# Optimization experiments

Measured on AMD Instinct MI355X. Metric: run time of the kernel, lower is better.

Reference implementation:

```python
import jax, jax.numpy as jnp
import numpy as np

QMAX = 127.0  # int8 symmetric range


def _quantize(t):
    # per-tensor symmetric int8 quantization
    scale = jnp.maximum(jnp.max(jnp.abs(t)) / QMAX, 1e-8)
    q = jnp.clip(jnp.round(t / scale), -QMAX, QMAX)
    return q, scale


def setup_inputs() -> dict:
    key = jax.random.key(0)
    kx, kw, kb = jax.random.split(key, 3)
    x = jax.random.normal(kx, (32, 128, 56, 56), dtype=jnp.float32)
    weight = jax.random.normal(kw, (256, 128, 3, 3), dtype=jnp.float32) * 0.05
    bias = jax.random.normal(kb, (256,), dtype=jnp.float32) * 0.05
    return {"x": x, "weight": weight, "bias": bias}


def reference(x, weight, bias):
    # Quantize activations and weights to int8 grid (values held in fp32;
    # products are exact small integers, matching int32 GEMM accumulation).
    qx, sx = _quantize(x)
    qw, sw = _quantize(weight)
    # im2col GEMM conv == standard conv on quantized values, int accumulate.
    acc = jax.lax.conv_general_dilated(
        qx, qw,
        window_strides=(1, 1),
        padding=((1, 1), (1, 1)),
        rhs_dilation=(1, 1),
        dimension_numbers=("NCHW", "OIHW", "NCHW"),
    )
    # Dequantize and add bias.
    out = acc * (sx * sw) + bias[None, :, None, None]
    return out
```

## Files before the change

### kernel.cpp

```cpp
#include <hip/hip_runtime.h>
#include <hip/hip_bf16.h>


typedef int v4i __attribute__((ext_vector_type(4)));

#define NBATCH 32
#define CIN    128
#define HW     56
#define PIX    (HW*HW)
#define COUT   256
#define XTOT   (NBATCH*CIN*PIX)
#define WTOT   (COUT*CIN*9)

template <int ITERS>
__global__ __launch_bounds__(256) void absmax_part_kernel(
    const float* __restrict__ in, float* __restrict__ partial)
{
    const float4* in4 = (const float4*)in;
    const int t      = blockIdx.x * 256 + threadIdx.x;
    const int stride = gridDim.x * 256;
    float m = 0.f;
#pragma unroll
    for (int k = 0; k < ITERS; ++k) {
        float4 v = in4[t + k * stride];
        m = fmaxf(m, fmaxf(fmaxf(fabsf(v.x), fabsf(v.y)),
                           fmaxf(fabsf(v.z), fabsf(v.w))));
    }
#pragma unroll
    for (int off = 32; off >= 1; off >>= 1)
        m = fmaxf(m, __shfl_xor(m, off, 64));
    __shared__ float wmax[4];
    const int lane = threadIdx.x & 63, wid = threadIdx.x >> 6;
    if (lane == 0) wmax[wid] = m;
    __syncthreads();
    if (threadIdx.x == 0)
        partial[blockIdx.x] =
            fmaxf(fmaxf(wmax[0], wmax[1]), fmaxf(wmax[2], wmax[3]));
}

__global__ __launch_bounds__(256) void finalize_kernel(
    const float* __restrict__ px, const float* __restrict__ pw,
    float* __restrict__ scales)
{
    const int tid = threadIdx.x;
    float mxv = 0.f, mwv = 0.f;
#pragma unroll
    for (int k = 0; k < 7; ++k)
        mxv = fmaxf(mxv, px[k * 256 + tid]);
    if (tid < 72) mwv = pw[tid];
#pragma unroll
    for (int off = 32; off >= 1; off >>= 1) {
        mxv = fmaxf(mxv, __shfl_xor(mxv, off, 64));
        mwv = fmaxf(mwv, __shfl_xor(mwv, off, 64));
    }
    __shared__ float sx[4], sw[4];
    const int lane = tid & 63, wid = tid >> 6;
    if (lane == 0) { sx[wid] = mxv; sw[wid] = mwv; }
    __syncthreads();
    if (tid == 0) {
        float fx = fmaxf(fmaxf(sx[0], sx[1]), fmaxf(sx[2], sx[3]));
        float fw = fmaxf(fmaxf(sw[0], sw[1]), fmaxf(sw[2], sw[3]));
        scales[0] = fmaxf(fx / 127.0f, 1e-8f);
        scales[1] = fmaxf(fw / 127.0f, 1e-8f);
    }
}

__global__ void quant_w_kernel(const float* __restrict__ w,
                               const float* __restrict__ scales,
                               signed char* __restrict__ qw) {
    float s = scales[1];
    int idx = blockIdx.x * blockDim.x + threadIdx.x;
    if (idx >= WTOT) return;
    int o   = idx / (CIN * 9);
    int rem = idx % (CIN * 9);
    int c   = rem / 9;
    int khw = rem % 9;
    float q = rintf(w[idx] / s);
    q = fminf(127.0f, fmaxf(-127.0f, q));
    qw[khw * (COUT * CIN) + o * CIN + c] = (signed char)(int)q;
}

__global__ __launch_bounds__(256) void quant_x_kernel(const float* __restrict__ x,
                                                      const float* __restrict__ scales,
                                                      signed char* __restrict__ qx) {
    __shared__ signed char lds[32 * 132];
    float s = scales[0];
    const int n   = blockIdx.y;
    const int p0  = blockIdx.x * 32;
    const int tid = threadIdx.x;
#pragma unroll
    for (int i = 0; i < 4; ++i) {
        int idx = i * 256 + tid;
        int c   = idx >> 3;
        int pq  = idx & 7;
        float4 v = *(const float4*)&x[((size_t)(n * CIN + c)) * PIX + p0 + pq * 4];
        float qv[4] = {v.x, v.y, v.z, v.w};
#pragma unroll
        for (int j = 0; j < 4; ++j) {
            float q = rintf(qv[j] / s);
            q = fminf(127.0f, fmaxf(-127.0f, q));
            lds[(pq * 4 + j) * 132 + c] = (signed char)(int)q;
        }
    }
    __syncthreads();
#pragma unroll
    for (int i = 0; i < 4; ++i) {
        int idx = i * 256 + tid;
        int pp  = idx >> 5;
        int cw  = (idx & 31) * 4;
        *(int*)&qx[((size_t)(n * PIX + p0 + pp)) * CIN + cw] =
            *(const int*)&lds[pp * 132 + cw];
    }
}

__global__ __launch_bounds__(256, 4) void conv_kernel(
    const signed char* __restrict__ qx,
    const signed char* __restrict__ qw,
    const float* __restrict__ bias,
    const float* __restrict__ scales,
    float* __restrict__ out)
{
    __shared__ signed char lds[232 * 128];
    const int tid  = threadIdx.x;
    const int lane = tid & 63;
    const int wid  = tid >> 6;
    const int prow = lane & 15;
    const int klo  = lane >> 4;

    const int bid = blockIdx.x;
    const int nh  = bid & 1;
    const int mt  = bid >> 1;
    const int n   = mt / 49;
    const int p0  = (mt % 49) * 64;
    const int hbase = p0 / HW - 1;

    const size_t xbase = (size_t)n * PIX * CIN;

#pragma unroll
    for (int it = 0; it < 8; ++it) {
        int chunk = it * 256 + tid;
        if (chunk < 232 * 8) {
            int r  = chunk >> 3;
            int cb = (chunk & 7) * 16;
            int hr = r / 58;
            int wc = r - hr * 58;
            int h  = hbase + hr;
            int w  = wc - 1;
            bool valid = ((unsigned)h < HW) && ((unsigned)w < HW);
            int p = valid ? (h * HW + w) : 0;
            v4i v = *(const v4i*)(qx + xbase + (size_t)p * CIN + cb);
            if (!valid) v = (v4i){0, 0, 0, 0};
            *(v4i*)&lds[r * 128 + (cb ^ ((r & 7) << 4))] = v;
        }
    }
    __syncthreads();

    int rr[4];
#pragma unroll
    for (int s = 0; s < 4; ++s) {
        int p = p0 + s * 16 + prow;
        int h = p / HW, w = p - h * HW;
        rr[s] = (h - hbase) * 58 + (w + 1);
    }

    const int ch0     = nh * 128 + wid * 32;
    const int colbase = klo * 16;

    v4i acc[4][2] = {};

    const signed char* b0ptr = qw + (size_t)(ch0 + prow) * CIN + colbase;
#define BADDR(st) (b0ptr + (size_t)((st) >> 1) * (COUT * CIN) + ((st) & 1) * 64)

    v4i bcur0 = *(const v4i*)BADDR(0);
    v4i bcur1 = *(const v4i*)(BADDR(0) + 16 * CIN);

#pragma unroll
    for (int st = 0; st < 18; ++st) {
        v4i bn0 = bcur0, bn1 = bcur1;
        if (st < 17) {
            const signed char* bp = BADDR(st + 1);
            bn0 = *(const v4i*)bp;
            bn1 = *(const v4i*)(bp + 16 * CIN);
        }
        const int khw  = st >> 1;
        const int rofs = (khw / 3 - 1) * 58 + (khw % 3 - 1);
        const int col  = (st & 1) * 64 + colbase;
        v4i a[4];
#pragma unroll
        for (int s = 0; s < 4; ++s) {
            int r = rr[s] + rofs;
            a[s] = *(const v4i*)&lds[r * 128 + (col ^ ((r & 7) << 4))];
        }
#pragma unroll
        for (int s = 0; s < 4; ++s) {
            acc[s][0] = __builtin_amdgcn_mfma_i32_16x16x64_i8(a[s], bcur0, acc[s][0], 0, 0, 0);
            acc[s][1] = __builtin_amdgcn_mfma_i32_16x16x64_i8(a[s], bcur1, acc[s][1], 0, 0, 0);
        }
        bcur0 = bn0; bcur1 = bn1;
    }
#undef BADDR

    float s0 = scales[0], s1 = scales[1];
    asm volatile("" : "+v"(s0));
    const float comb = s0 * s1;
    const size_t obase = (size_t)n * COUT * PIX;
#pragma unroll
    for (int t = 0; t < 2; ++t) {
        int ch = ch0 + t * 16 + prow;
        float bs = bias[ch];
#pragma unroll
        for (int s = 0; s < 4; ++s) {
            int p = p0 + s * 16 + klo * 4;
            float4 v;
            v.x = (float)acc[s][t].x * comb + bs;
            v.y = (float)acc[s][t].y * comb + bs;
            v.z = (float)acc[s][t].z * comb + bs;
            v.w = (float)acc[s][t].w * comb + bs;
            *(float4*)&out[obase + (size_t)ch * PIX + p] = v;
        }
    }
}

extern "C" void kernel_launch(void* const* d_in, const int* in_sizes, int n_in,
                              void* d_out, int out_size, void* d_ws, size_t ws_size,
                              hipStream_t stream) {
    const float* x    = (const float*)d_in[0];
    const float* w    = (const float*)d_in[1];
    const float* bias = (const float*)d_in[2];
    float* out = (float*)d_out;

    float*       scales = (float*)d_ws;
    float*       px     = (float*)((char*)d_ws + 256);
    float*       pw     = (float*)((char*)d_ws + 7680);
    signed char* qx     = (signed char*)d_ws + 8192;
    signed char* qw     = qx + (size_t)XTOT;

    absmax_part_kernel<7><<<1792, 256, 0, stream>>>(x, px);
    absmax_part_kernel<4><<<72, 256, 0, stream>>>(w, pw);
    finalize_kernel<<<1, 256, 0, stream>>>(px, pw, scales);
    quant_w_kernel<<<WTOT / 256, 256, 0, stream>>>(w, scales, qw);
    quant_x_kernel<<<dim3(98, 32), 256, 0, stream>>>(x, scales, qx);
    conv_kernel<<<3136, 256, 0, stream>>>(qx, qw, bias, scales, out);
}
```

Baseline: 217.9 us.

## Widen conv tile to all 256 output channels and merge absmax launches

Each conv block now computes all 256 output channels for its 64-pixel tile instead of half, so the staged input halo in LDS is loaded once rather than twice and the grid halves. Blocks are remapped with a stride-8 swizzle across the 1568 tiles. The two absmax reductions are merged into one launch, saving a kernel launch. The wider tile doubles accumulator registers (16 MFMA accumulators per wave) and drops the B-operand software prefetch, which may cut occupancy under the 4-block launch bound and expose global load latency.

```diff
diff --git a/kernel.cpp b/kernel.cpp
--- a/kernel.cpp
+++ b/kernel.cpp
@@ -12,19 +12,32 @@
 #define XTOT   (NBATCH*CIN*PIX)
 #define WTOT   (COUT*CIN*9)
 
-template <int ITERS>
-__global__ __launch_bounds__(256) void absmax_part_kernel(
-    const float* __restrict__ in, float* __restrict__ partial)
+__global__ __launch_bounds__(256) void absmax_both_kernel(
+    const float* __restrict__ x, const float* __restrict__ w,
+    float* __restrict__ px, float* __restrict__ pw)
 {
-    const float4* in4 = (const float4*)in;
-    const int t      = blockIdx.x * 256 + threadIdx.x;
-    const int stride = gridDim.x * 256;
+    const int bid = blockIdx.x;
     float m = 0.f;
-#pragma unroll
-    for (int k = 0; k < ITERS; ++k) {
-        float4 v = in4[t + k * stride];
-        m = fmaxf(m, fmaxf(fmaxf(fabsf(v.x), fabsf(v.y)),
-                           fmaxf(fabsf(v.z), fabsf(v.w))));
+    if (bid < 1792) {
+        const float4* in4 = (const float4*)x;
+        const int t = bid * 256 + threadIdx.x;
+        const int stride = 1792 * 256;
+#pragma unroll
+        for (int k = 0; k < 7; ++k) {
+            float4 v = in4[t + k * stride];
+            m = fmaxf(m, fmaxf(fmaxf(fabsf(v.x), fabsf(v.y)),
+                               fmaxf(fabsf(v.z), fabsf(v.w))));
+        }
+    } else {
+        const float4* in4 = (const float4*)w;
+        const int t = (bid - 1792) * 256 + threadIdx.x;
+        const int stride = 72 * 256;
+#pragma unroll
+        for (int k = 0; k < 4; ++k) {
+            float4 v = in4[t + k * stride];
+            m = fmaxf(m, fmaxf(fmaxf(fabsf(v.x), fabsf(v.y)),
+                               fmaxf(fabsf(v.z), fabsf(v.w))));
+        }
     }
 #pragma unroll
     for (int off = 32; off >= 1; off >>= 1)
@@ -33,9 +46,10 @@
     const int lane = threadIdx.x & 63, wid = threadIdx.x >> 6;
     if (lane == 0) wmax[wid] = m;
     __syncthreads();
-    if (threadIdx.x == 0)
-        partial[blockIdx.x] =
-            fmaxf(fmaxf(wmax[0], wmax[1]), fmaxf(wmax[2], wmax[3]));
+    if (threadIdx.x == 0) {
+        float r = fmaxf(fmaxf(wmax[0], wmax[1]), fmaxf(wmax[2], wmax[3]));
+        if (bid < 1792) px[bid] = r; else pw[bid - 1792] = r;
+    }
 }
 
 __global__ __launch_bounds__(256) void finalize_kernel(
@@ -127,11 +141,9 @@
     const int prow = lane & 15;
     const int klo  = lane >> 4;
 
-    const int bid = blockIdx.x;
-    const int nh  = bid & 1;
-    const int mt  = bid >> 1;
-    const int n   = mt / 49;
-    const int p0  = (mt % 49) * 64;
+    const int bid = (blockIdx.x & 7) * 196 + (blockIdx.x >> 3);
+    const int n   = bid / 49;
+    const int p0  = (bid % 49) * 64;
     const int hbase = p0 / HW - 1;
 
     const size_t xbase = (size_t)n * PIX * CIN;
@@ -163,49 +175,45 @@
         rr[s] = (h - hbase) * 58 + (w + 1);
     }
 
-    const int ch0     = nh * 128 + wid * 32;
+    const int ch0     = wid * 64;
     const int colbase = klo * 16;
 
-    v4i acc[4][2] = {};
+    v4i acc[4][4] = {};
 
     const signed char* b0ptr = qw + (size_t)(ch0 + prow) * CIN + colbase;
-#define BADDR(st) (b0ptr + (size_t)((st) >> 1) * (COUT * CIN) + ((st) & 1) * 64)
-
-    v4i bcur0 = *(const v4i*)BADDR(0);
-    v4i bcur1 = *(const v4i*)(BADDR(0) + 16 * CIN);
-
-#pragma unroll
-    for (int st = 0; st < 18; ++st) {
-        v4i bn0 = bcur0, bn1 = bcur1;
-        if (st < 17) {
-            const signed char* bp = BADDR(st + 1);
-            bn0 = *(const v4i*)bp;
-            bn1 = *(const v4i*)(bp + 16 * CIN);
-        }
-        const int khw  = st >> 1;
+
+#pragma unroll
+    for (int khw = 0; khw < 9; ++khw) {
         const int rofs = (khw / 3 - 1) * 58 + (khw % 3 - 1);
-        const int col  = (st & 1) * 64 + colbase;
-        v4i a[4];
-#pragma unroll
-        for (int s = 0; s < 4; ++s) {
-            int r = rr[s] + rofs;
-            a[s] = *(const v4i*)&lds[r * 128 + (col ^ ((r & 7) << 4))];
-        }
-#pragma unroll
-        for (int s = 0; s < 4; ++s) {
-            acc[s][0] = __builtin_amdgcn_mfma_i32_16x16x64_i8(a[s], bcur0, acc[s][0], 0, 0, 0);
-            acc[s][1] = __builtin_amdgcn_mfma_i32_16x16x64_i8(a[s], bcur1, acc[s][1], 0, 0, 0);
-        }
-        bcur0 = bn0; bcur1 = bn1;
-    }
-#undef BADDR
+        const signed char* bk = b0ptr + (size_t)khw * (COUT * CIN);
+#pragma unroll
+        for (int kc = 0; kc < 2; ++kc) {
+            v4i b[4];
+#pragma unroll
+            for (int t = 0; t < 4; ++t)
+                b[t] = *(const v4i*)(bk + kc * 64 + (size_t)t * 16 * CIN);
+            const int col = kc * 64 + colbase;
+            v4i a[4];
+#pragma unroll
+            for (int s = 0; s < 4; ++s) {
+                int r = rr[s] + rofs;
+                a[s] = *(const v4i*)&lds[r * 128 + (col ^ ((r & 7) << 4))];
+            }
+#pragma unroll
+            for (int s = 0; s < 4; ++s)
+#pragma unroll
+                for (int t = 0; t < 4; ++t)
+                    acc[s][t] = __builtin_amdgcn_mfma_i32_16x16x64_i8(
+                        a[s], b[t], acc[s][t], 0, 0, 0);
+        }
+    }
 
     float s0 = scales[0], s1 = scales[1];
     asm volatile("" : "+v"(s0));
     const float comb = s0 * s1;
     const size_t obase = (size_t)n * COUT * PIX;
 #pragma unroll
-    for (int t = 0; t < 2; ++t) {
+    for (int t = 0; t < 4; ++t) {
         int ch = ch0 + t * 16 + prow;
         float bs = bias[ch];
 #pragma unroll
@@ -235,10 +243,9 @@
     signed char* qx     = (signed char*)d_ws + 8192;
     signed char* qw     = qx + (size_t)XTOT;
 
-    absmax_part_kernel<7><<<1792, 256, 0, stream>>>(x, px);
-    absmax_part_kernel<4><<<72, 256, 0, stream>>>(w, pw);
+    absmax_both_kernel<<<1864, 256, 0, stream>>>(x, w, px, pw);
     finalize_kernel<<<1, 256, 0, stream>>>(px, pw, scales);
     quant_w_kernel<<<WTOT / 256, 256, 0, stream>>>(w, scales, qw);
     quant_x_kernel<<<dim3(98, 32), 256, 0, stream>>>(x, scales, qx);
-    conv_kernel<<<3136, 256, 0, stream>>>(qx, qw, bias, scales, out);
-}
+    conv_kernel<<<1568, 256, 0, stream>>>(qx, qw, bias, scales, out);
+}
```

Result: slower. 255.8 us (+17.4%).
